# Performance work log

Measured on AMD Instinct MI355X. Metric: run time of the kernel, lower is better.

## Reference

```python
import jax, jax.numpy as jnp
import numpy as np

B, FIN, H, W = 16, 256, 32, 32
NH, FH = 8, 64
CIN = FIN + 2  # fin + 2 coordinate-grid pos channels
COUT = NH * FH


def setup_inputs() -> dict:
    key = jax.random.key(0)
    ks = jax.random.split(key, 9)
    s = 1.0 / np.sqrt(CIN)
    so = 1.0 / np.sqrt(COUT)
    return {
        "x": jax.random.normal(ks[0], (B, FIN, H, W), dtype=jnp.float32),
        "wq": jax.random.uniform(ks[1], (COUT, CIN), jnp.float32, -s, s),
        "bq": jax.random.uniform(ks[2], (COUT,), jnp.float32, -s, s),
        "wk": jax.random.uniform(ks[3], (COUT, CIN), jnp.float32, -s, s),
        "bk": jax.random.uniform(ks[4], (COUT,), jnp.float32, -s, s),
        "wv": jax.random.uniform(ks[5], (COUT, CIN), jnp.float32, -s, s),
        "bv": jax.random.uniform(ks[6], (COUT,), jnp.float32, -s, s),
        "wo": jax.random.uniform(ks[7], (FIN, COUT), jnp.float32, -so, so),
        "bo": jax.random.uniform(ks[8], (FIN,), jnp.float32, -so, so),
    }


def reference(x, wq, bq, wk, bk, wv, bv, wo, bo):
    b, c, h, w = x.shape
    n = h * w
    # PosEncoding: concat one linspace(-1,1) coordinate channel per spatial dim
    gy, gx = jnp.meshgrid(jnp.linspace(-1.0, 1.0, h), jnp.linspace(-1.0, 1.0, w), indexing="ij")
    pos = jnp.broadcast_to(jnp.stack([gy, gx])[None], (b, 2, h, w)).astype(x.dtype)
    t = jnp.concatenate([x, pos], axis=1).reshape(b, c + 2, n)  # [B, C+2, N]
    # 1x1 convs are per-token GEMMs
    q = (jnp.einsum("oc,bcn->bon", wq, t) + bq[:, None]).reshape(b, NH, FH, n)
    k = (jnp.einsum("oc,bcn->bon", wk, t) + bk[:, None]).reshape(b, NH, FH, n)
    v = (jnp.einsum("oc,bcn->bon", wv, t) + bv[:, None]).reshape(b, NH, FH, n)
    temp = FH ** 0.5
    attn = jax.nn.softmax(jnp.einsum("bhdn,bhdm->bhnm", q, k) / temp, axis=-1)
    o = jnp.einsum("bhnm,bhdm->bhdn", attn, v).reshape(b, NH * FH, n)
    o = jnp.einsum("oc,bcn->bon", wo, o) + bo[:, None]
    return x + o.reshape(b, c, h, w)
```

## Files before the change

kernel.cpp:

```cpp
#include <hip/hip_runtime.h>


typedef unsigned short u16;
typedef unsigned int   u32;
typedef __attribute__((ext_vector_type(8))) short  short8;
typedef __attribute__((ext_vector_type(4))) float  float4_;

#define MFMA16(a, b, c) __builtin_amdgcn_mfma_f32_16x16x32_bf16(a, b, c, 0, 0, 0)

__device__ __forceinline__ float bf2f(u16 u) {
    union { u32 i; float f; } v; v.i = ((u32)u) << 16; return v.f;
}
__device__ __forceinline__ u16 f2bf(float f) {
    union { float f; u32 i; } v; v.f = f;
    u32 r = v.i + 0x7FFFu + ((v.i >> 16) & 1u);
    return (u16)(r >> 16);
}
__device__ __forceinline__ float exp2_fast(float x) {
    float r;
    asm("v_exp_f32 %0, %1" : "=v"(r) : "v"(x));
    return r;
}
__device__ __forceinline__ u32 cvtpk_bf16(float lo, float hi) {
    u32 r;
    asm("v_cvt_pk_bf16_f32 %0, %1, %2" : "=v"(r) : "v"(lo), "v"(hi));
    return r;
}

__global__ __launch_bounds__(256) void prep(
    const float* __restrict__ wq, const float* __restrict__ wk,
    const float* __restrict__ wv, const float* __restrict__ x,
    u16* __restrict__ wb, u16* __restrict__ xT)
{
    __shared__ float Lt[64][65];
    const int bid = blockIdx.x;
    const int tid = threadIdx.x;
    if (bid < 512) {
        int i = bid * 256 + tid;
        int o = i >> 8, c = i & 255;
        size_t si = (size_t)o * 258 + c;
        wb[i]          = f2bf(wq[si]);
        wb[131072 + i] = f2bf(wk[si]);
        wb[262144 + i] = f2bf(wv[si]);
    } else {
        int r = bid - 512;
        int n0 = (r & 15) * 64, c0 = ((r >> 4) & 3) * 64, b = r >> 6;
#pragma unroll
        for (int p = 0; p < 4; ++p) {
            int c = p * 16 + (tid >> 4);
            int nn = (tid & 15) * 4;
            float4 v = *(const float4*)&x[((size_t)(b * 256) + c0 + c) * 1024 + n0 + nn];
            Lt[c][nn + 0] = v.x; Lt[c][nn + 1] = v.y;
            Lt[c][nn + 2] = v.z; Lt[c][nn + 3] = v.w;
        }
        __syncthreads();
#pragma unroll
        for (int p = 0; p < 4; ++p) {
            int n = p * 16 + (tid >> 4);
            int cc = (tid & 15) * 4;
            ushort4 st;
            st.x = f2bf(Lt[cc + 0][n]); st.y = f2bf(Lt[cc + 1][n]);
            st.z = f2bf(Lt[cc + 2][n]); st.w = f2bf(Lt[cc + 3][n]);
            *(ushort4*)&xT[((size_t)(b << 10) + n0 + n) * 256 + c0 + cc] = st;
        }
    }
}

__global__ __launch_bounds__(256) void qkv_mfma(
    const u16* __restrict__ xT, const u16* __restrict__ wb,
    const float* __restrict__ wq, const float* __restrict__ wk,
    const float* __restrict__ wv,
    const float* __restrict__ bq, const float* __restrict__ bk,
    const float* __restrict__ bv,
    u16* __restrict__ qkvbuf)
{
    __shared__ u16 Wl[128 * 64];
    __shared__ u16 Tl[128 * 64];
    const int tid = threadIdx.x;
    const int lane = tid & 63, w = tid >> 6;
    const int quad = lane >> 4, m15 = lane & 15;
    const int n0 = blockIdx.x * 128, mt = blockIdx.y, b = blockIdx.z;
    const int mat = mt >> 2;
    const int m0 = mt * 128;
    const float* worig = (mat == 0) ? wq : ((mat == 1) ? wk : wv);
    const float* bias  = (mat == 0) ? bq : ((mat == 1) ? bk : bv);
    const float oscale = (mat == 1) ? 0.1803368801111204f : 1.0f;
    u16* outbuf = qkvbuf + (size_t)mat * 8388608;

    float4_ acc[2][8];
#pragma unroll
    for (int s = 0; s < 2; ++s)
#pragma unroll
        for (int t = 0; t < 8; ++t) acc[s][t] = (float4_){0, 0, 0, 0};

    const int srow = tid >> 2;
    const int sc8  = (tid & 3) * 8;
    const int rdsw = (m15 & 7) << 3;
    const int sw0  = (srow & 7) << 3;

    const u16* wsrc = wb + (size_t)(m0 + srow) * 256 + sc8;
    const u16* tsrc = xT + ((size_t)(b << 10) + n0 + srow) * 256 + sc8;

    {
        short8 w0 = *(const short8*)(wsrc);
        short8 w1 = *(const short8*)(wsrc + 64 * 256);
        short8 t0 = *(const short8*)(tsrc);
        short8 t1 = *(const short8*)(tsrc + 64 * 256);
        *(short8*)&Wl[srow * 64 + (sc8 ^ sw0)]        = w0;
        *(short8*)&Wl[(srow + 64) * 64 + (sc8 ^ sw0)] = w1;
        *(short8*)&Tl[srow * 64 + (sc8 ^ sw0)]        = t0;
        *(short8*)&Tl[(srow + 64) * 64 + (sc8 ^ sw0)] = t1;
    }
    __syncthreads();

#pragma unroll
    for (int k = 0; k < 8; ++k) {
        const int p = k & 1;
        short8 pw0, pw1, pt0, pt1;
        if (k < 7) {
            const int kc = (k + 1) * 32;
            pw0 = *(const short8*)(wsrc + kc);
            pw1 = *(const short8*)(wsrc + 64 * 256 + kc);
            pt0 = *(const short8*)(tsrc + kc);
            pt1 = *(const short8*)(tsrc + 64 * 256 + kc);
        }

        const int cb = p * 32 + quad * 8;
        short8 af0 = *(const short8*)&Wl[(w * 32 + m15) * 64 + (cb ^ rdsw)];
        short8 af1 = *(const short8*)&Wl[(w * 32 + 16 + m15) * 64 + (cb ^ rdsw)];
        __builtin_amdgcn_s_setprio(1);
#pragma unroll
        for (int t = 0; t < 8; ++t) {
            short8 bf = *(const short8*)&Tl[(t * 16 + m15) * 64 + (cb ^ rdsw)];
            acc[0][t] = MFMA16(af0, bf, acc[0][t]);
            acc[1][t] = MFMA16(af1, bf, acc[1][t]);
        }
        __builtin_amdgcn_s_setprio(0);

        if (k < 7) {
            const int pc = (p ^ 1) * 32 + sc8;
            *(short8*)&Wl[srow * 64 + (pc ^ sw0)]        = pw0;
            *(short8*)&Wl[(srow + 64) * 64 + (pc ^ sw0)] = pw1;
            *(short8*)&Tl[srow * 64 + (pc ^ sw0)]        = pt0;
            *(short8*)&Tl[(srow + 64) * 64 + (pc ^ sw0)] = pt1;
        }
        __syncthreads();
    }

#pragma unroll
    for (int s = 0; s < 2; ++s) {
        float wg[4], wx[4], bi[4];
#pragma unroll
        for (int r = 0; r < 4; ++r) {
            int om = (mt & 3) * 128 + w * 32 + s * 16 + quad * 4 + r;
            wg[r] = worig[(size_t)om * 258 + 256];
            wx[r] = worig[(size_t)om * 258 + 257];
            bi[r] = bias[om];
        }
        const int h = (mt & 3) * 2 + ((w * 32 + s * 16) >> 6);
        const int dbase = ((w * 32 + s * 16) & 63) + quad * 4;
#pragma unroll
        for (int t = 0; t < 8; ++t) {
            int n = n0 + t * 16 + m15;
            float gy = -1.0f + 2.0f * (float)(n >> 5) / 31.0f;
            float gx = -1.0f + 2.0f * (float)(n & 31) / 31.0f;
            float v[4];
#pragma unroll
            for (int r = 0; r < 4; ++r)
                v[r] = (acc[s][t][r] + wg[r] * gy + wx[r] * gx + bi[r]) * oscale;
            if (mat != 2) {
                ushort4 st;
                st.x = f2bf(v[0]); st.y = f2bf(v[1]);
                st.z = f2bf(v[2]); st.w = f2bf(v[3]);
                *(ushort4*)&outbuf[((size_t)(b * 8 + h) * 1024 + n) * 64 + dbase] = st;
            } else {
#pragma unroll
                for (int r = 0; r < 4; ++r)
                    outbuf[((size_t)(b * 8 + h) * 64 + dbase + r) * 1024 + n] = f2bf(v[r]);
            }
        }
    }
}

__global__ __launch_bounds__(512) void attn_mfma(
    u16* __restrict__ qbuf, const u16* __restrict__ kbuf,
    const u16* __restrict__ vbuf)
{
    __shared__ u16 Kl[64 * 64];
    __shared__ u16 Vl[64 * 64];
    __shared__ u16 Pl[8][8][16][8];

    const int tid = threadIdx.x;
    const int lane = tid & 63, w = tid >> 6;
    const int quad = lane >> 4, m15 = lane & 15;
    const int bh = blockIdx.x;
    const int q0 = blockIdx.y * 128;
    u16* qb = qbuf + (size_t)bh * 65536;
    const u16* kb = kbuf + (size_t)bh * 65536;
    const u16* vb = vbuf + (size_t)bh * 65536;

    short8 qf[2];
    {
        const u16* qr = qb + (size_t)(q0 + w * 16 + m15) * 64 + quad * 8;
        qf[0] = *(const short8*)qr;
        qf[1] = *(const short8*)(qr + 32);
    }

    float4_ O[4];
    float lp = 0.0f;
#pragma unroll
    for (int t = 0; t < 4; ++t) O[t] = (float4_){0, 0, 0, 0};

    const int row = tid >> 3, c8 = (tid & 7) * 8;
    const int stsw = c8 ^ ((row & 7) << 3);
    const int rdsw = (m15 & 7) << 3;

    {
        short8 k0 = *(const short8*)(kb + (size_t)row * 64 + c8);
        short8 v0 = *(const short8*)(vb + (size_t)row * 1024 + c8);
        *(short8*)&Kl[row * 64 + stsw] = k0;
        *(short8*)&Vl[row * 64 + stsw] = v0;
    }
    __syncthreads();

    short8 kr, vr;
    for (int kt0 = 0; kt0 < 1024; kt0 += 64) {
        const bool more = (kt0 < 960);
        if (more) {
            kr = *(const short8*)(kb + (size_t)(kt0 + 64 + row) * 64 + c8);
            vr = *(const short8*)(vb + (size_t)row * 1024 + kt0 + 64 + c8);
        }

        float4_ S[4];
#pragma unroll
        for (int t = 0; t < 4; ++t) S[t] = (float4_){0, 0, 0, 0};
#pragma unroll
        for (int c = 0; c < 2; ++c) {
            short8 kf[4];
#pragma unroll
            for (int t = 0; t < 4; ++t)
                kf[t] = *(const short8*)&Kl[(t * 16 + m15) * 64 +
                                            ((c * 32 + quad * 8) ^ rdsw)];
            __builtin_amdgcn_s_setprio(1);
#pragma unroll
            for (int t = 0; t < 4; ++t)
                S[t] = MFMA16(kf[t], qf[c], S[t]);
            __builtin_amdgcn_s_setprio(0);
        }

        {
            float lsum = 0.0f;
#pragma unroll
            for (int t = 0; t < 4; ++t) {
                float p0 = exp2_fast(S[t][0]);
                float p1 = exp2_fast(S[t][1]);
                float p2 = exp2_fast(S[t][2]);
                float p3 = exp2_fast(S[t][3]);
                uint2 st; st.x = cvtpk_bf16(p0, p1); st.y = cvtpk_bf16(p2, p3);
                *(uint2*)&Pl[w][t * 2 + (quad >> 1)][m15][(quad & 1) * 4] = st;
                lsum += (p0 + p1) + (p2 + p3);
            }
            lp += lsum;
        }

#pragma unroll
        for (int c = 0; c < 2; ++c) {
            short8 av[4];
#pragma unroll
            for (int dt = 0; dt < 4; ++dt)
                av[dt] = *(const short8*)&Vl[(dt * 16 + m15) * 64 +
                                             ((c * 32 + quad * 8) ^ rdsw)];
            short8 bp = *(const short8*)&Pl[w][c * 4 + quad][m15][0];
            __builtin_amdgcn_s_setprio(1);
#pragma unroll
            for (int dt = 0; dt < 4; ++dt)
                O[dt] = MFMA16(av[dt], bp, O[dt]);
            __builtin_amdgcn_s_setprio(0);
        }

        __syncthreads();
        if (more) {
            *(short8*)&Kl[row * 64 + stsw] = kr;
            *(short8*)&Vl[row * 64 + stsw] = vr;
            __syncthreads();
        }
    }

    {
        float v = lp;
        v += __shfl_xor(v, 16);
        v += __shfl_xor(v, 32);
        float linv = 1.0f / v;
        int n = q0 + w * 16 + m15;
#pragma unroll
        for (int dt = 0; dt < 4; ++dt) {
            ushort4 st;
            st.x = f2bf(O[dt][0] * linv);
            st.y = f2bf(O[dt][1] * linv);
            st.z = f2bf(O[dt][2] * linv);
            st.w = f2bf(O[dt][3] * linv);
            *(ushort4*)&qb[(size_t)n * 64 + dt * 16 + quad * 4] = st;
        }
    }
}

__global__ __launch_bounds__(256) void proj_mfma(
    const u16* __restrict__ ao, const float* __restrict__ wo,
    const float* __restrict__ bo, const float* __restrict__ x,
    float* __restrict__ out)
{
    __shared__ u16 Wl[64 * 64];
    __shared__ u16 Tl[64 * 64];
    const int tid = threadIdx.x;
    const int lane = tid & 63, w = tid >> 6;
    const int quad = lane >> 4, m15 = lane & 15;
    const int n0 = blockIdx.x * 64, f0 = blockIdx.y * 64, b = blockIdx.z;

    float4_ acc[4] = {{0,0,0,0},{0,0,0,0},{0,0,0,0},{0,0,0,0}};
    const int row = tid >> 3, c8 = (tid & 7) * 8;
    const int stsw = c8 ^ ((row & 7) << 3);
    const int rdsw = (m15 & 7) << 3;

    for (int cc0 = 0; cc0 < 512; cc0 += 64) {
        __syncthreads();
        const int h = cc0 >> 6;
#pragma unroll
        for (int rr = 0; rr < 64; rr += 32) {
            const float* wsrc = wo + (size_t)(f0 + row + rr) * 512 + cc0 + c8;
            float4 v0 = *(const float4*)wsrc;
            float4 v1 = *(const float4*)(wsrc + 4);
            uint4 pk;
            pk.x = cvtpk_bf16(v0.x, v0.y);
            pk.y = cvtpk_bf16(v0.z, v0.w);
            pk.z = cvtpk_bf16(v1.x, v1.y);
            pk.w = cvtpk_bf16(v1.z, v1.w);
            *(uint4*)&Wl[(row + rr) * 64 + stsw] = pk;
            *(short8*)&Tl[(row + rr) * 64 + stsw] =
                *(const short8*)(ao + ((size_t)((b << 3) + h) * 1024 + n0 + row + rr) * 64 + c8);
        }
        __syncthreads();
#pragma unroll
        for (int c = 0; c < 2; ++c) {
            short8 af = *(const short8*)&Wl[(w * 16 + m15) * 64 +
                                            ((c * 32 + quad * 8) ^ rdsw)];
#pragma unroll
            for (int t = 0; t < 4; ++t) {
                short8 bf = *(const short8*)&Tl[(t * 16 + m15) * 64 +
                                                ((c * 32 + quad * 8) ^ rdsw)];
                acc[t] = MFMA16(af, bf, acc[t]);
            }
        }
    }

    float bi[4];
#pragma unroll
    for (int r = 0; r < 4; ++r) bi[r] = bo[f0 + w * 16 + quad * 4 + r];
#pragma unroll
    for (int t = 0; t < 4; ++t) {
        int n = n0 + t * 16 + m15;
#pragma unroll
        for (int r = 0; r < 4; ++r) {
            int f = f0 + w * 16 + quad * 4 + r;
            size_t idx = ((size_t)(b * 256) + f) * 1024 + n;
            out[idx] = acc[t][r] + bi[r] + x[idx];
        }
    }
}

extern "C" void kernel_launch(void* const* d_in, const int* in_sizes, int n_in,
                              void* d_out, int out_size, void* d_ws, size_t ws_size,
                              hipStream_t stream) {
    const float* x  = (const float*)d_in[0];
    const float* wq = (const float*)d_in[1];
    const float* bq = (const float*)d_in[2];
    const float* wk = (const float*)d_in[3];
    const float* bk = (const float*)d_in[4];
    const float* wv = (const float*)d_in[5];
    const float* bv = (const float*)d_in[6];
    const float* wo = (const float*)d_in[7];
    const float* bo = (const float*)d_in[8];

    u16* qkvbuf = (u16*)d_ws;
    u16* region = qkvbuf + 3 * 8388608;
    u16* xT = region;
    u16* wb = region + 4194304;

    prep<<<1536, 256, 0, stream>>>(wq, wk, wv, x, wb, xT);

    qkv_mfma<<<dim3(8, 12, 16), 256, 0, stream>>>(
        xT, wb, wq, wk, wv, bq, bk, bv, qkvbuf);

    attn_mfma<<<dim3(128, 8), 512, 0, stream>>>(
        qkvbuf, qkvbuf + 8388608, qkvbuf + 16777216);

    proj_mfma<<<dim3(16, 4, 16), 256, 0, stream>>>(qkvbuf, wo, bo, x, (float*)d_out);
}
```

Baseline: 174.3 us.

## Process two query subtiles per wave in attention to double K/V reuse

Each wave in the attention kernel now handles 32 queries (two 16-row subtiles) rather than 16, so each block covers 256 queries and the grid's query dimension is halved. Every K/V tile staged in shared memory therefore feeds twice as many MFMAs, which cuts global K/V traffic and LDS staging per query. The register prefetch of the next K/V tile is also dropped in favour of a plain synchronous load with a barrier on each side. This raises register pressure and halves the block count to 512, which risks lower occupancy and exposes load latency.

```diff
diff --git a/kernel.cpp b/kernel.cpp
--- a/kernel.cpp
+++ b/kernel.cpp
@@ -188,52 +188,49 @@
 {
     __shared__ u16 Kl[64 * 64];
     __shared__ u16 Vl[64 * 64];
-    __shared__ u16 Pl[8][8][16][8];
+    __shared__ u16 Pl[8][2][8][16][8];
 
     const int tid = threadIdx.x;
     const int lane = tid & 63, w = tid >> 6;
     const int quad = lane >> 4, m15 = lane & 15;
     const int bh = blockIdx.x;
-    const int q0 = blockIdx.y * 128;
+    const int q0 = blockIdx.y * 256;
     u16* qb = qbuf + (size_t)bh * 65536;
     const u16* kb = kbuf + (size_t)bh * 65536;
     const u16* vb = vbuf + (size_t)bh * 65536;
 
-    short8 qf[2];
-    {
-        const u16* qr = qb + (size_t)(q0 + w * 16 + m15) * 64 + quad * 8;
-        qf[0] = *(const short8*)qr;
-        qf[1] = *(const short8*)(qr + 32);
-    }
-
-    float4_ O[4];
-    float lp = 0.0f;
-#pragma unroll
-    for (int t = 0; t < 4; ++t) O[t] = (float4_){0, 0, 0, 0};
+    short8 qf[2][2];
+#pragma unroll
+    for (int s = 0; s < 2; ++s) {
+        const u16* qr = qb + (size_t)(q0 + w * 32 + s * 16 + m15) * 64 + quad * 8;
+        qf[s][0] = *(const short8*)qr;
+        qf[s][1] = *(const short8*)(qr + 32);
+    }
+
+    float4_ O[2][4];
+    float lp[2] = {0.0f, 0.0f};
+#pragma unroll
+    for (int s = 0; s < 2; ++s)
+#pragma unroll
+        for (int t = 0; t < 4; ++t) O[s][t] = (float4_){0, 0, 0, 0};
 
     const int row = tid >> 3, c8 = (tid & 7) * 8;
     const int stsw = c8 ^ ((row & 7) << 3);
     const int rdsw = (m15 & 7) << 3;
 
-    {
-        short8 k0 = *(const short8*)(kb + (size_t)row * 64 + c8);
-        short8 v0 = *(const short8*)(vb + (size_t)row * 1024 + c8);
-        *(short8*)&Kl[row * 64 + stsw] = k0;
-        *(short8*)&Vl[row * 64 + stsw] = v0;
-    }
-    __syncthreads();
-
-    short8 kr, vr;
     for (int kt0 = 0; kt0 < 1024; kt0 += 64) {
-        const bool more = (kt0 < 960);
-        if (more) {
-            kr = *(const short8*)(kb + (size_t)(kt0 + 64 + row) * 64 + c8);
-            vr = *(const short8*)(vb + (size_t)row * 1024 + kt0 + 64 + c8);
-        }
-
-        float4_ S[4];
-#pragma unroll
-        for (int t = 0; t < 4; ++t) S[t] = (float4_){0, 0, 0, 0};
+        __syncthreads();
+        *(short8*)&Kl[row * 64 + stsw] =
+            *(const short8*)(kb + (size_t)(kt0 + row) * 64 + c8);
+        *(short8*)&Vl[row * 64 + stsw] =
+            *(const short8*)(vb + (size_t)row * 1024 + kt0 + c8);
+        __syncthreads();
+
+        float4_ S[2][4];
+#pragma unroll
+        for (int s = 0; s < 2; ++s)
+#pragma unroll
+            for (int t = 0; t < 4; ++t) S[s][t] = (float4_){0, 0, 0, 0};
 #pragma unroll
         for (int c = 0; c < 2; ++c) {
             short8 kf[4];
@@ -243,24 +240,27 @@
                                             ((c * 32 + quad * 8) ^ rdsw)];
             __builtin_amdgcn_s_setprio(1);
 #pragma unroll
-            for (int t = 0; t < 4; ++t)
-                S[t] = MFMA16(kf[t], qf[c], S[t]);
+            for (int s = 0; s < 2; ++s)
+#pragma unroll
+                for (int t = 0; t < 4; ++t)
+                    S[s][t] = MFMA16(kf[t], qf[s][c], S[s][t]);
             __builtin_amdgcn_s_setprio(0);
         }
 
-        {
+#pragma unroll
+        for (int s = 0; s < 2; ++s) {
             float lsum = 0.0f;
 #pragma unroll
             for (int t = 0; t < 4; ++t) {
-                float p0 = exp2_fast(S[t][0]);
-                float p1 = exp2_fast(S[t][1]);
-                float p2 = exp2_fast(S[t][2]);
-                float p3 = exp2_fast(S[t][3]);
+                float p0 = exp2_fast(S[s][t][0]);
+                float p1 = exp2_fast(S[s][t][1]);
+                float p2 = exp2_fast(S[s][t][2]);
+                float p3 = exp2_fast(S[s][t][3]);
                 uint2 st; st.x = cvtpk_bf16(p0, p1); st.y = cvtpk_bf16(p2, p3);
-                *(uint2*)&Pl[w][t * 2 + (quad >> 1)][m15][(quad & 1) * 4] = st;
+                *(uint2*)&Pl[w][s][t * 2 + (quad >> 1)][m15][(quad & 1) * 4] = st;
                 lsum += (p0 + p1) + (p2 + p3);
             }
-            lp += lsum;
+            lp[s] += lsum;
         }
 
 #pragma unroll
@@ -270,35 +270,32 @@
             for (int dt = 0; dt < 4; ++dt)
                 av[dt] = *(const short8*)&Vl[(dt * 16 + m15) * 64 +
                                              ((c * 32 + quad * 8) ^ rdsw)];
-            short8 bp = *(const short8*)&Pl[w][c * 4 + quad][m15][0];
-            __builtin_amdgcn_s_setprio(1);
-#pragma unroll
-            for (int dt = 0; dt < 4; ++dt)
-                O[dt] = MFMA16(av[dt], bp, O[dt]);
-            __builtin_amdgcn_s_setprio(0);
-        }
-
-        __syncthreads();
-        if (more) {
-            *(short8*)&Kl[row * 64 + stsw] = kr;
-            *(short8*)&Vl[row * 64 + stsw] = vr;
-            __syncthreads();
-        }
-    }
-
-    {
-        float v = lp;
+#pragma unroll
+            for (int s = 0; s < 2; ++s) {
+                short8 bp = *(const short8*)&Pl[w][s][c * 4 + quad][m15][0];
+                __builtin_amdgcn_s_setprio(1);
+#pragma unroll
+                for (int dt = 0; dt < 4; ++dt)
+                    O[s][dt] = MFMA16(av[dt], bp, O[s][dt]);
+                __builtin_amdgcn_s_setprio(0);
+            }
+        }
+    }
+
+#pragma unroll
+    for (int s = 0; s < 2; ++s) {
+        float v = lp[s];
         v += __shfl_xor(v, 16);
         v += __shfl_xor(v, 32);
         float linv = 1.0f / v;
-        int n = q0 + w * 16 + m15;
+        int n = q0 + w * 32 + s * 16 + m15;
 #pragma unroll
         for (int dt = 0; dt < 4; ++dt) {
             ushort4 st;
-            st.x = f2bf(O[dt][0] * linv);
-            st.y = f2bf(O[dt][1] * linv);
-            st.z = f2bf(O[dt][2] * linv);
-            st.w = f2bf(O[dt][3] * linv);
+            st.x = f2bf(O[s][dt][0] * linv);
+            st.y = f2bf(O[s][dt][1] * linv);
+            st.z = f2bf(O[s][dt][2] * linv);
+            st.w = f2bf(O[s][dt][3] * linv);
             *(ushort4*)&qb[(size_t)n * 64 + dt * 16 + quad * 4] = st;
         }
     }
@@ -390,7 +387,7 @@
     qkv_mfma<<<dim3(8, 12, 16), 256, 0, stream>>>(
         xT, wb, wq, wk, wv, bq, bk, bv, qkvbuf);
 
-    attn_mfma<<<dim3(128, 8), 512, 0, stream>>>(
+    attn_mfma<<<dim3(128, 4), 512, 0, stream>>>(
         qkvbuf, qkvbuf + 8388608, qkvbuf + 16777216);
 
     proj_mfma<<<dim3(16, 4, 16), 256, 0, stream>>>(qkvbuf, wo, bo, x, (float*)d_out);
```

Result: faster. 164.0 us (-5.9%).
